# Kernel tuning notes

Hardware: AMD Instinct MI355X
Metric: run time of the kernel (lower is better)

The kernel has to match this reference:

```python
import jax, jax.numpy as jnp
import numpy as np
from jax import lax

B, CHI, CHO, H, W = 8, 128, 128, 64, 64
K = 3
KK = K * K


def setup_inputs() -> dict:
    key = jax.random.key(0)
    ks = jax.random.split(key, 7)
    x = jax.random.normal(ks[0], (B, CHI, H, W), jnp.float32)
    # small offset-conv weights so sampled offsets stay in a realistic few-pixel range
    off_w = jax.random.normal(ks[1], (3 * KK, CHI, K, K), jnp.float32) * 0.01
    off_b = jnp.zeros((3 * KK,), jnp.float32)
    w = jax.random.normal(ks[2], (CHO, CHI, K, K), jnp.float32) / np.sqrt(CHI * KK).astype(np.float32)
    b = jnp.zeros((CHO,), jnp.float32)
    gamma = jax.random.uniform(ks[3], (CHO,), jnp.float32)  # nn.init.uniform_ on BN weight
    beta = jnp.zeros((CHO,), jnp.float32)
    return {"x": x, "off_w": off_w, "off_b": off_b, "w": w, "b": b, "gamma": gamma, "beta": beta}


def _deform_conv(x, off_w, off_b, w, b):
    """DCNv2 modulated deformable conv, k=3, stride=1, pad=1, dil=1, 1 deform group."""
    B_, C, H_, W_ = x.shape
    # offset/mask branch: plain 3x3 conv -> 27 channels (2*9 offsets, 9 masks)
    om = lax.conv_general_dilated(x, off_w, (1, 1), ((1, 1), (1, 1)),
                                  dimension_numbers=("NCHW", "OIHW", "NCHW"))
    om = om + off_b[None, :, None, None]
    off = om[:, : 2 * KK].reshape(B_, KK, 2, H_, W_)  # [B,9,2,H,W]; ch 2k=y, 2k+1=x
    mask = jax.nn.sigmoid(om[:, 2 * KK:])             # [B,9,H,W]

    ky, kx = jnp.meshgrid(jnp.arange(K, dtype=jnp.float32),
                          jnp.arange(K, dtype=jnp.float32), indexing="ij")
    ky = ky.reshape(KK); kx = kx.reshape(KK)
    # sampling positions: p = p0 - pad + k*dil + offset
    py = off[:, :, 0] + (jnp.arange(H_, dtype=jnp.float32) - 1.0)[None, None, :, None] + ky[None, :, None, None]
    px = off[:, :, 1] + (jnp.arange(W_, dtype=jnp.float32) - 1.0)[None, None, None, :] + kx[None, :, None, None]

    y0 = jnp.floor(py); x0 = jnp.floor(px)
    ly = py - y0; lx = px - x0
    xf = x.reshape(B_, C, H_ * W_)

    def corner(yi, xi, wgt):
        valid = ((yi >= 0) & (yi <= H_ - 1) & (xi >= 0) & (xi <= W_ - 1)).astype(x.dtype)
        yc = jnp.clip(yi, 0, H_ - 1).astype(jnp.int32)
        xc = jnp.clip(xi, 0, W_ - 1).astype(jnp.int32)
        idx = (yc * W_ + xc).reshape(B_, KK * H_ * W_)
        g = jax.vmap(lambda xb, ib: xb[:, ib])(xf, idx).reshape(B_, C, KK, H_, W_)
        return g * (valid * wgt)[:, None]

    val = (corner(y0, x0, (1 - ly) * (1 - lx))
           + corner(y0, x0 + 1, (1 - ly) * lx)
           + corner(y0 + 1, x0, ly * (1 - lx))
           + corner(y0 + 1, x0 + 1, ly * lx))  # [B,C,9,H,W]
    val = val * mask[:, None]  # modulation
    out = jnp.einsum("bckhw,ock->bohw", val, w.reshape(w.shape[0], C, KK))
    return out + b[None, :, None, None]


def reference(x, off_w, off_b, w, b, gamma, beta):
    y = _deform_conv(x, off_w, off_b, w, b)
    # BatchNorm2d in training mode (batch statistics), eps=1e-5, then ReLU
    mean = y.mean(axis=(0, 2, 3))
    var = y.var(axis=(0, 2, 3))
    yn = (y - mean[None, :, None, None]) * lax.rsqrt(var[None, :, None, None] + 1e-5)
    return jax.nn.relu(yn * gamma[None, :, None, None] + beta[None, :, None, None])
```

## Files before the change

kernel.cpp:

```cpp
#include <hip/hip_runtime.h>
#include <hip/hip_bf16.h>
#include <math.h>

#define HH 64
#define WW 64
#define HW 4096
#define LDV 136

typedef __bf16 bf16x8 __attribute__((ext_vector_type(8)));
typedef float floatx4 __attribute__((ext_vector_type(4)));
typedef unsigned int uint4a __attribute__((ext_vector_type(4)));
typedef unsigned int uint2a __attribute__((ext_vector_type(2)));

#define WS_Y    0u
#define WS_PSQ  16777216u
#define WS_XTB  16778240u
#define WS_WTB  25166848u
#define WS_OWB  25461760u

static __device__ inline ushort f2bf(float f) {
  __hip_bfloat16 h = __float2bfloat16(f);
  return __builtin_bit_cast(ushort, h);
}
static __device__ inline float lo16(unsigned int u) { return __builtin_bit_cast(float, u << 16); }
static __device__ inline float hi16(unsigned int u) { return __builtin_bit_cast(float, u & 0xffff0000u); }

__global__ __launch_bounds__(256) void k_prepw(const float* __restrict__ w,
                                               const float* __restrict__ ow,
                                               ushort* __restrict__ wtb,
                                               ushort* __restrict__ owb) {
  int idx = blockIdx.x * 256 + threadIdx.x;
  if (idx < 147456) {
    int c = idx & 127, o = (idx >> 7) & 127, k = idx >> 14;
    wtb[idx] = f2bf(w[(o * 128 + c) * 9 + k]);
  } else {
    int j = idx - 147456;
    if (j < 36864) {
      int c = j & 127, o = (j >> 7) & 31, k = j >> 12;
      float v = (o < 27) ? ow[(o * 128 + c) * 9 + k] : 0.f;
      owb[j] = f2bf(v);
    }
  }
}

__global__ __launch_bounds__(256) void k_xt(const float* __restrict__ x,
                                            ushort* __restrict__ xtb) {
  __shared__ float tile[32][33];
  int hw0 = blockIdx.x * 32;
  int c0 = blockIdx.y * 32;
  int b = blockIdx.z;
  int col = threadIdx.x & 31, row = threadIdx.x >> 5;
  const float* xb = x + ((size_t)b * 128 + c0) * HW + hw0;
#pragma unroll
  for (int i = 0; i < 32; i += 8)
    tile[row + i][col] = xb[(size_t)(row + i) * HW + col];
  __syncthreads();
  int hw = threadIdx.x >> 3, cq = threadIdx.x & 7;
  ushort* xo = xtb + ((size_t)b * HW + hw0) * 128 + c0;
  unsigned int lo = (unsigned int)f2bf(tile[cq * 4 + 0][hw]) |
                    ((unsigned int)f2bf(tile[cq * 4 + 1][hw]) << 16);
  unsigned int hi = (unsigned int)f2bf(tile[cq * 4 + 2][hw]) |
                    ((unsigned int)f2bf(tile[cq * 4 + 3][hw]) << 16);
  uint2a v2 = (uint2a){lo, hi};
  *(uint2a*)(&xo[(size_t)hw * 128 + cq * 4]) = v2;
}

__global__ __launch_bounds__(256) void k_main(
    const ushort* __restrict__ xtb, const ushort* __restrict__ wtb,
    const ushort* __restrict__ owb, const float* __restrict__ off_b,
    const float* __restrict__ bias, float* __restrict__ y) {
  __shared__ ushort Vl[32 * LDV];
  __shared__ float omL[27 * 32];
  int t = threadIdx.x;
  int lane = t & 63, wv = t >> 6;
  int li = lane & 15, quad = lane >> 4;
  int hr = blockIdx.x;
  int row = hr >> 1, p0b = (hr & 1) * 32;
  int b = blockIdx.y;
  const ushort* xb = xtb + (size_t)b * HW * 128;
  int ch = t & 15;
  int pq = t >> 4;

  int mi = wv & 1, ni = wv >> 1;
  floatx4 oacc = (floatx4){0.f, 0.f, 0.f, 0.f};
  uint4a u0, u1;
  auto p1load = [&](int k, int p, uint4a& u) {
    int ky = k / 3, kx = k % 3;
    int ry = row - 1 + ky, cx = p0b + p - 1 + kx;
    bool v = (ry >= 0 && ry < HH && cx >= 0 && cx < WW);
    int idx = v ? (ry * WW + cx) : 0;
    uint4a a = *(const uint4a*)(xb + (size_t)idx * 128 + ch * 8);
    u = v ? a : (uint4a){0u, 0u, 0u, 0u};
  };
  p1load(0, pq, u0);
  p1load(0, pq + 16, u1);
  for (int k = 0; k < 9; ++k) {
    __syncthreads();
    *(uint4a*)(&Vl[pq * LDV + ch * 8]) = u0;
    *(uint4a*)(&Vl[(pq + 16) * LDV + ch * 8]) = u1;
    if (k < 8) {
      p1load(k + 1, pq, u0);
      p1load(k + 1, pq + 16, u1);
    }
    __syncthreads();
#pragma unroll
    for (int ks = 0; ks < 4; ++ks) {
      bf16x8 bfrag = __builtin_bit_cast(bf16x8,
          *(const uint4a*)(&Vl[(ni * 16 + li) * LDV + ks * 32 + quad * 8]));
      bf16x8 afrag = __builtin_bit_cast(bf16x8,
          *(const uint4a*)(&owb[(size_t)(k * 32 + mi * 16 + li) * 128 + ks * 32 + quad * 8]));
      oacc = __builtin_amdgcn_mfma_f32_16x16x32_bf16(afrag, bfrag, oacc, 0, 0, 0);
    }
  }
#pragma unroll
  for (int r = 0; r < 4; ++r) {
    int o = mi * 16 + quad * 4 + r;
    if (o < 27) omL[o * 32 + ni * 16 + li] = oacc[r] + off_b[o];
  }
  __syncthreads();

  floatx4 macc[2][2];
#pragma unroll
  for (int i = 0; i < 2; ++i)
#pragma unroll
    for (int j = 0; j < 2; ++j) macc[i][j] = (floatx4){0.f, 0.f, 0.f, 0.f};

  float wqA[4], wqB[4];
  int idxA[4], idxB[4];
  uint4a u[8];

  auto prep = [&](int k, int p, float* wq, int* idx4) {
    int ky = k / 3, kx = k % 3;
    float offy = omL[(2 * k) * 32 + p];
    float offx = omL[(2 * k + 1) * 32 + p];
    float mraw = omL[(18 + k) * 32 + p];
    float m = 1.f / (1.f + __expf(-mraw));
    float py = offy + (float)(row - 1 + ky);
    float px = offx + (float)(p0b + p - 1 + kx);
    float y0f = floorf(py), x0f = floorf(px);
    float ly = py - y0f, lx = px - x0f;
    int iy0 = (int)y0f, ix0 = (int)x0f;
    int iy1 = iy0 + 1, ix1 = ix0 + 1;
    float w00 = (1.f - ly) * (1.f - lx) * m, w01 = (1.f - ly) * lx * m;
    float w10 = ly * (1.f - lx) * m, w11 = ly * lx * m;
    if (iy0 < 0 || iy0 > HH - 1) { w00 = 0.f; w01 = 0.f; }
    if (iy1 < 0 || iy1 > HH - 1) { w10 = 0.f; w11 = 0.f; }
    if (ix0 < 0 || ix0 > WW - 1) { w00 = 0.f; w10 = 0.f; }
    if (ix1 < 0 || ix1 > WW - 1) { w01 = 0.f; w11 = 0.f; }
    int cy0 = min(max(iy0, 0), HH - 1), cy1 = min(max(iy1, 0), HH - 1);
    int cx0 = min(max(ix0, 0), WW - 1), cx1 = min(max(ix1, 0), WW - 1);
    idx4[0] = cy0 * WW + cx0;
    idx4[1] = cy0 * WW + cx1;
    idx4[2] = cy1 * WW + cx0;
    idx4[3] = cy1 * WW + cx1;
    wq[0] = w00; wq[1] = w01; wq[2] = w10; wq[3] = w11;
  };
  auto issue = [&]() {
#pragma unroll
    for (int c = 0; c < 4; ++c)
      u[c] = *(const uint4a*)(xb + (size_t)idxA[c] * 128 + ch * 8);
#pragma unroll
    for (int c = 0; c < 4; ++c)
      u[4 + c] = *(const uint4a*)(xb + (size_t)idxB[c] * 128 + ch * 8);
  };

  prep(0, pq, wqA, idxA);
  prep(0, pq + 16, wqB, idxB);
  issue();
  for (int k = 0; k < 9; ++k) {
    __syncthreads();
    {
      uint4a outv;
#pragma unroll
      for (int e = 0; e < 4; ++e) {
        float rlo = wqA[0] * lo16(u[0][e]) + wqA[1] * lo16(u[1][e]) +
                    wqA[2] * lo16(u[2][e]) + wqA[3] * lo16(u[3][e]);
        float rhi = wqA[0] * hi16(u[0][e]) + wqA[1] * hi16(u[1][e]) +
                    wqA[2] * hi16(u[2][e]) + wqA[3] * hi16(u[3][e]);
        outv[e] = (unsigned int)f2bf(rlo) | ((unsigned int)f2bf(rhi) << 16);
      }
      *(uint4a*)(&Vl[pq * LDV + ch * 8]) = outv;
    }
    {
      uint4a outv;
#pragma unroll
      for (int e = 0; e < 4; ++e) {
        float rlo = wqB[0] * lo16(u[4][e]) + wqB[1] * lo16(u[5][e]) +
                    wqB[2] * lo16(u[6][e]) + wqB[3] * lo16(u[7][e]);
        float rhi = wqB[0] * hi16(u[4][e]) + wqB[1] * hi16(u[5][e]) +
                    wqB[2] * hi16(u[6][e]) + wqB[3] * hi16(u[7][e]);
        outv[e] = (unsigned int)f2bf(rlo) | ((unsigned int)f2bf(rhi) << 16);
      }
      *(uint4a*)(&Vl[(pq + 16) * LDV + ch * 8]) = outv;
    }
    if (k < 8) {
      prep(k + 1, pq, wqA, idxA);
      prep(k + 1, pq + 16, wqB, idxB);
      issue();
    }
    __syncthreads();
    const ushort* Arow = &wtb[(size_t)(k * 128 + wv * 32) * 128];
#pragma unroll
    for (int ks = 0; ks < 4; ++ks) {
      bf16x8 b0 = __builtin_bit_cast(bf16x8,
          *(const uint4a*)(&Vl[(li)*LDV + ks * 32 + quad * 8]));
      bf16x8 b1 = __builtin_bit_cast(bf16x8,
          *(const uint4a*)(&Vl[(16 + li) * LDV + ks * 32 + quad * 8]));
      bf16x8 a0 = __builtin_bit_cast(bf16x8,
          *(const uint4a*)(Arow + (size_t)(li)*128 + ks * 32 + quad * 8));
      bf16x8 a1 = __builtin_bit_cast(bf16x8,
          *(const uint4a*)(Arow + (size_t)(16 + li) * 128 + ks * 32 + quad * 8));
      macc[0][0] = __builtin_amdgcn_mfma_f32_16x16x32_bf16(a0, b0, macc[0][0], 0, 0, 0);
      macc[0][1] = __builtin_amdgcn_mfma_f32_16x16x32_bf16(a0, b1, macc[0][1], 0, 0, 0);
      macc[1][0] = __builtin_amdgcn_mfma_f32_16x16x32_bf16(a1, b0, macc[1][0], 0, 0, 0);
      macc[1][1] = __builtin_amdgcn_mfma_f32_16x16x32_bf16(a1, b1, macc[1][1], 0, 0, 0);
    }
  }
#pragma unroll
  for (int ot = 0; ot < 2; ++ot)
#pragma unroll
    for (int pt = 0; pt < 2; ++pt)
#pragma unroll
      for (int r = 0; r < 4; ++r) {
        int o = wv * 32 + ot * 16 + quad * 4 + r;
        int p = p0b + pt * 16 + li;
        y[((size_t)(b * 128 + o)) * HW + row * 64 + p] = macc[ot][pt][r] + bias[o];
      }
}

__global__ __launch_bounds__(256) void k_stats(const float* __restrict__ y,
                                               float* __restrict__ psq) {
  int o = blockIdx.x, b = blockIdx.y, t = threadIdx.x;
  const float4* yb = (const float4*)(y + ((size_t)(b * 128 + o)) * HW);
  float s = 0.f, q = 0.f;
#pragma unroll
  for (int i = 0; i < 4; ++i) {
    float4 v = yb[t + i * 256];
    s += v.x + v.y + v.z + v.w;
    q += v.x * v.x + v.y * v.y + v.z * v.z + v.w * v.w;
  }
#pragma unroll
  for (int off = 32; off >= 1; off >>= 1) {
    s += __shfl_down(s, off, 64);
    q += __shfl_down(q, off, 64);
  }
  __shared__ float bs[4], bq[4];
  if ((t & 63) == 0) { bs[t >> 6] = s; bq[t >> 6] = q; }
  __syncthreads();
  if (t == 0) {
    atomicAdd(&psq[o], bs[0] + bs[1] + bs[2] + bs[3]);
    atomicAdd(&psq[128 + o], bq[0] + bq[1] + bq[2] + bq[3]);
  }
}

__global__ __launch_bounds__(256) void k_norm(const float* __restrict__ y,
                                              const float* __restrict__ psq,
                                              const float* __restrict__ gamma,
                                              const float* __restrict__ beta,
                                              float* __restrict__ out) {
  int blk = blockIdx.x;
  int o = (blk >> 2) & 127;
  float s = psq[o], q = psq[128 + o];
  float mean = s * (1.f / 32768.f);
  float var = q * (1.f / 32768.f) - mean * mean;
  float scale = gamma[o] * rsqrtf(var + 1e-5f);
  float shift = beta[o] - mean * scale;
  int i4 = blk * 256 + threadIdx.x;
  float4 v = ((const float4*)y)[i4];
  float4 r;
  r.x = fmaxf(v.x * scale + shift, 0.f);
  r.y = fmaxf(v.y * scale + shift, 0.f);
  r.z = fmaxf(v.z * scale + shift, 0.f);
  r.w = fmaxf(v.w * scale + shift, 0.f);
  ((float4*)out)[i4] = r;
}

extern "C" void kernel_launch(void* const* d_in, const int* in_sizes, int n_in,
                              void* d_out, int out_size, void* d_ws, size_t ws_size,
                              hipStream_t stream) {
  const float* x     = (const float*)d_in[0];
  const float* off_w = (const float*)d_in[1];
  const float* off_b = (const float*)d_in[2];
  const float* w     = (const float*)d_in[3];
  const float* bias  = (const float*)d_in[4];
  const float* gamma = (const float*)d_in[5];
  const float* beta  = (const float*)d_in[6];
  float* out = (float*)d_out;
  char* ws = (char*)d_ws;

  float* y    = (float*)(ws + WS_Y);
  float* psq  = (float*)(ws + WS_PSQ);
  ushort* xtb = (ushort*)(ws + WS_XTB);
  ushort* wtb = (ushort*)(ws + WS_WTB);
  ushort* owb = (ushort*)(ws + WS_OWB);

  hipMemsetAsync(psq, 0, 256 * sizeof(float), stream);
  k_prepw<<<720, 256, 0, stream>>>(w, off_w, wtb, owb);
  k_xt<<<dim3(128, 4, 8), 256, 0, stream>>>(x, xtb);
  k_main<<<dim3(128, 8), 256, 0, stream>>>(xtb, wtb, owb, off_b, bias, y);
  k_stats<<<dim3(128, 8), 256, 0, stream>>>(y, psq);
  k_norm<<<4096, 256, 0, stream>>>(y, psq, gamma, beta, out);
}
```

Baseline: 161.1 us.

## Fuse prep kernels, fold BN statistics into main kernel epilogue, prefetch weights

Merges the x-transpose and the two weight-conversion kernels into one launch, which also zeroes the stats buffer in place of the memset. Computes the per-channel sum and sum of squares in the main kernel's epilogue with shuffles and atomics, which removes the separate stats pass that re-read y. Also loads the weight fragments for each tap before the interpolation step so their global latency overlaps that work. In exchange there are many more atomics, and the extra register pressure from the prefetched fragments may hurt occupancy.

After: 233.3 us. +44.8%, slower.

```diff
diff --git a/kernel.cpp b/kernel.cpp
--- a/kernel.cpp
+++ b/kernel.cpp
@@ -25,50 +25,52 @@
 static __device__ inline float lo16(unsigned int u) { return __builtin_bit_cast(float, u << 16); }
 static __device__ inline float hi16(unsigned int u) { return __builtin_bit_cast(float, u & 0xffff0000u); }
 
-__global__ __launch_bounds__(256) void k_prepw(const float* __restrict__ w,
-                                               const float* __restrict__ ow,
-                                               ushort* __restrict__ wtb,
-                                               ushort* __restrict__ owb) {
-  int idx = blockIdx.x * 256 + threadIdx.x;
-  if (idx < 147456) {
+__global__ __launch_bounds__(256) void k_prep(const float* __restrict__ x,
+                                              const float* __restrict__ w,
+                                              const float* __restrict__ ow,
+                                              ushort* __restrict__ xtb,
+                                              ushort* __restrict__ wtb,
+                                              ushort* __restrict__ owb,
+                                              float* __restrict__ psq) {
+  __shared__ float tile[32][33];
+  int bid = blockIdx.x;
+  if (bid < 4096) {
+    int hw0 = (bid & 127) * 32;
+    int c0 = ((bid >> 7) & 3) * 32;
+    int b = bid >> 9;
+    int col = threadIdx.x & 31, row = threadIdx.x >> 5;
+    const float* xb = x + ((size_t)b * 128 + c0) * HW + hw0;
+#pragma unroll
+    for (int i = 0; i < 32; i += 8)
+      tile[row + i][col] = xb[(size_t)(row + i) * HW + col];
+    __syncthreads();
+    int hw = threadIdx.x >> 3, cq = threadIdx.x & 7;
+    ushort* xo = xtb + ((size_t)b * HW + hw0) * 128 + c0;
+    unsigned int lo = (unsigned int)f2bf(tile[cq * 4 + 0][hw]) |
+                      ((unsigned int)f2bf(tile[cq * 4 + 1][hw]) << 16);
+    unsigned int hi = (unsigned int)f2bf(tile[cq * 4 + 2][hw]) |
+                      ((unsigned int)f2bf(tile[cq * 4 + 3][hw]) << 16);
+    uint2a v2 = (uint2a){lo, hi};
+    *(uint2a*)(&xo[(size_t)hw * 128 + cq * 4]) = v2;
+  } else if (bid < 4096 + 576) {
+    int idx = (bid - 4096) * 256 + threadIdx.x;
     int c = idx & 127, o = (idx >> 7) & 127, k = idx >> 14;
     wtb[idx] = f2bf(w[(o * 128 + c) * 9 + k]);
+  } else if (bid < 4096 + 720) {
+    int j = (bid - 4672) * 256 + threadIdx.x;
+    int c = j & 127, o = (j >> 7) & 31, k = j >> 12;
+    float v = (o < 27) ? ow[(o * 128 + c) * 9 + k] : 0.f;
+    owb[j] = f2bf(v);
   } else {
-    int j = idx - 147456;
-    if (j < 36864) {
-      int c = j & 127, o = (j >> 7) & 31, k = j >> 12;
-      float v = (o < 27) ? ow[(o * 128 + c) * 9 + k] : 0.f;
-      owb[j] = f2bf(v);
-    }
-  }
-}
-
-__global__ __launch_bounds__(256) void k_xt(const float* __restrict__ x,
-                                            ushort* __restrict__ xtb) {
-  __shared__ float tile[32][33];
-  int hw0 = blockIdx.x * 32;
-  int c0 = blockIdx.y * 32;
-  int b = blockIdx.z;
-  int col = threadIdx.x & 31, row = threadIdx.x >> 5;
-  const float* xb = x + ((size_t)b * 128 + c0) * HW + hw0;
-#pragma unroll
-  for (int i = 0; i < 32; i += 8)
-    tile[row + i][col] = xb[(size_t)(row + i) * HW + col];
-  __syncthreads();
-  int hw = threadIdx.x >> 3, cq = threadIdx.x & 7;
-  ushort* xo = xtb + ((size_t)b * HW + hw0) * 128 + c0;
-  unsigned int lo = (unsigned int)f2bf(tile[cq * 4 + 0][hw]) |
-                    ((unsigned int)f2bf(tile[cq * 4 + 1][hw]) << 16);
-  unsigned int hi = (unsigned int)f2bf(tile[cq * 4 + 2][hw]) |
-                    ((unsigned int)f2bf(tile[cq * 4 + 3][hw]) << 16);
-  uint2a v2 = (uint2a){lo, hi};
-  *(uint2a*)(&xo[(size_t)hw * 128 + cq * 4]) = v2;
+    psq[threadIdx.x] = 0.f;
+  }
 }
 
 __global__ __launch_bounds__(256) void k_main(
     const ushort* __restrict__ xtb, const ushort* __restrict__ wtb,
     const ushort* __restrict__ owb, const float* __restrict__ off_b,
-    const float* __restrict__ bias, float* __restrict__ y) {
+    const float* __restrict__ bias, float* __restrict__ y,
+    float* __restrict__ psq) {
   __shared__ ushort Vl[32 * LDV];
   __shared__ float omL[27 * 32];
   int t = threadIdx.x;
@@ -169,6 +171,13 @@
   issue();
   for (int k = 0; k < 9; ++k) {
     __syncthreads();
+    const ushort* Arow = &wtb[(size_t)(k * 128 + wv * 32) * 128];
+    uint4a af[8];
+#pragma unroll
+    for (int ks = 0; ks < 4; ++ks) {
+      af[ks * 2] = *(const uint4a*)(Arow + (size_t)(li)*128 + ks * 32 + quad * 8);
+      af[ks * 2 + 1] = *(const uint4a*)(Arow + (size_t)(16 + li) * 128 + ks * 32 + quad * 8);
+    }
     {
       uint4a outv;
 #pragma unroll
@@ -199,17 +208,14 @@
       issue();
     }
     __syncthreads();
-    const ushort* Arow = &wtb[(size_t)(k * 128 + wv * 32) * 128];
 #pragma unroll
     for (int ks = 0; ks < 4; ++ks) {
       bf16x8 b0 = __builtin_bit_cast(bf16x8,
           *(const uint4a*)(&Vl[(li)*LDV + ks * 32 + quad * 8]));
       bf16x8 b1 = __builtin_bit_cast(bf16x8,
           *(const uint4a*)(&Vl[(16 + li) * LDV + ks * 32 + quad * 8]));
-      bf16x8 a0 = __builtin_bit_cast(bf16x8,
-          *(const uint4a*)(Arow + (size_t)(li)*128 + ks * 32 + quad * 8));
-      bf16x8 a1 = __builtin_bit_cast(bf16x8,
-          *(const uint4a*)(Arow + (size_t)(16 + li) * 128 + ks * 32 + quad * 8));
+      bf16x8 a0 = __builtin_bit_cast(bf16x8, af[ks * 2]);
+      bf16x8 a1 = __builtin_bit_cast(bf16x8, af[ks * 2 + 1]);
       macc[0][0] = __builtin_amdgcn_mfma_f32_16x16x32_bf16(a0, b0, macc[0][0], 0, 0, 0);
       macc[0][1] = __builtin_amdgcn_mfma_f32_16x16x32_bf16(a0, b1, macc[0][1], 0, 0, 0);
       macc[1][0] = __builtin_amdgcn_mfma_f32_16x16x32_bf16(a1, b0, macc[1][0], 0, 0, 0);
@@ -219,38 +225,27 @@
 #pragma unroll
   for (int ot = 0; ot < 2; ++ot)
 #pragma unroll
-    for (int pt = 0; pt < 2; ++pt)
-#pragma unroll
-      for (int r = 0; r < 4; ++r) {
-        int o = wv * 32 + ot * 16 + quad * 4 + r;
+    for (int r = 0; r < 4; ++r) {
+      int o = wv * 32 + ot * 16 + quad * 4 + r;
+      float s = 0.f, q = 0.f;
+#pragma unroll
+      for (int pt = 0; pt < 2; ++pt) {
         int p = p0b + pt * 16 + li;
-        y[((size_t)(b * 128 + o)) * HW + row * 64 + p] = macc[ot][pt][r] + bias[o];
-      }
-}
-
-__global__ __launch_bounds__(256) void k_stats(const float* __restrict__ y,
-                                               float* __restrict__ psq) {
-  int o = blockIdx.x, b = blockIdx.y, t = threadIdx.x;
-  const float4* yb = (const float4*)(y + ((size_t)(b * 128 + o)) * HW);
-  float s = 0.f, q = 0.f;
-#pragma unroll
-  for (int i = 0; i < 4; ++i) {
-    float4 v = yb[t + i * 256];
-    s += v.x + v.y + v.z + v.w;
-    q += v.x * v.x + v.y * v.y + v.z * v.z + v.w * v.w;
-  }
-#pragma unroll
-  for (int off = 32; off >= 1; off >>= 1) {
-    s += __shfl_down(s, off, 64);
-    q += __shfl_down(q, off, 64);
-  }
-  __shared__ float bs[4], bq[4];
-  if ((t & 63) == 0) { bs[t >> 6] = s; bq[t >> 6] = q; }
-  __syncthreads();
-  if (t == 0) {
-    atomicAdd(&psq[o], bs[0] + bs[1] + bs[2] + bs[3]);
-    atomicAdd(&psq[128 + o], bq[0] + bq[1] + bq[2] + bq[3]);
-  }
+        float val = macc[ot][pt][r] + bias[o];
+        y[((size_t)(b * 128 + o)) * HW + row * 64 + p] = val;
+        s += val;
+        q += val * val;
+      }
+#pragma unroll
+      for (int off = 8; off >= 1; off >>= 1) {
+        s += __shfl_down(s, off, 16);
+        q += __shfl_down(q, off, 16);
+      }
+      if (li == 0) {
+        atomicAdd(&psq[o], s);
+        atomicAdd(&psq[128 + o], q);
+      }
+    }
 }
 
 __global__ __launch_bounds__(256) void k_norm(const float* __restrict__ y,
@@ -294,10 +289,7 @@
   ushort* wtb = (ushort*)(ws + WS_WTB);
   ushort* owb = (ushort*)(ws + WS_OWB);
 
-  hipMemsetAsync(psq, 0, 256 * sizeof(float), stream);
-  k_prepw<<<720, 256, 0, stream>>>(w, off_w, wtb, owb);
-  k_xt<<<dim3(128, 4, 8), 256, 0, stream>>>(x, xtb);
-  k_main<<<dim3(128, 8), 256, 0, stream>>>(xtb, wtb, owb, off_b, bias, y);
-  k_stats<<<dim3(128, 8), 256, 0, stream>>>(y, psq);
+  k_prep<<<4817, 256, 0, stream>>>(x, w, off_w, xtb, wtb, owb, psq);
+  k_main<<<dim3(128, 8), 256, 0, stream>>>(xtb, wtb, owb, off_b, bias, y, psq);
   k_norm<<<4096, 256, 0, stream>>>(y, psq, gamma, beta, out);
 }
```
